# Optimization experiments

Measured on AMD Instinct MI355X. Metric: run time of the kernel, lower is better.

## Reference

```python
import jax, jax.numpy as jnp
import numpy as np

N_NODES = 100000
N_EDGES = 3200000
D_IN = 128
D_OUT = 128
LN_EPS = 1e-5


def setup_inputs() -> dict:
    key = jax.random.key(0)
    k1, k2, k3, k4 = jax.random.split(key, 4)
    x = jax.random.normal(k1, (N_NODES, D_IN), dtype=jnp.float32)
    edge_index = jax.random.randint(k2, (2, N_EDGES), 0, N_NODES, dtype=jnp.int64)
    edge_weight = jax.random.uniform(k3, (N_EDGES,), dtype=jnp.float32)
    W = jax.random.normal(k4, (D_IN, D_OUT), dtype=jnp.float32) * (1.0 / np.sqrt(D_IN))
    b = jnp.zeros((D_OUT,), dtype=jnp.float32)
    gamma = jnp.ones((D_OUT,), dtype=jnp.float32)
    beta = jnp.zeros((D_OUT,), dtype=jnp.float32)
    return {"x": x, "edge_index": edge_index, "edge_weight": edge_weight,
            "W": W, "b": b, "gamma": gamma, "beta": beta}


def _gcn_layer(x, edge_index, edge_weight, W, b, gamma, beta):
    n = x.shape[0]
    row, col = edge_index[0], edge_index[1]  # source -> target
    # add self-loops with weight 1 (PyG GCNConv default)
    loop = jnp.arange(n, dtype=edge_index.dtype)
    row_f = jnp.concatenate([row, loop])
    col_f = jnp.concatenate([col, loop])
    w_f = jnp.concatenate([edge_weight, jnp.ones((n,), dtype=edge_weight.dtype)])
    # symmetric normalization: deg^-1/2[row] * w * deg^-1/2[col]
    deg = jax.ops.segment_sum(w_f, col_f, num_segments=n)
    dis = jnp.where(deg > 0, jax.lax.rsqrt(jnp.maximum(deg, 1e-30)), 0.0)
    norm = dis[row_f] * w_f * dis[col_f]  # [E+N]
    # linear transform first (cheaper), then gather/scatter-add over edges
    h = x @ W  # [N, D_OUT]
    msgs = norm[:, None] * h[row_f]  # [E+N, D_OUT]
    agg = jax.ops.segment_sum(msgs, col_f, num_segments=n) + b
    # LayerNorm over features
    mu = jnp.mean(agg, axis=-1, keepdims=True)
    var = jnp.mean(jnp.square(agg - mu), axis=-1, keepdims=True)
    normed = (agg - mu) * jax.lax.rsqrt(var + LN_EPS) * gamma + beta
    # ReLU; dropout is identity in eval mode
    return jax.nn.relu(normed)


def reference(x, edge_index, edge_weight, W, b, gamma, beta):
    return _gcn_layer(x, edge_index, edge_weight, W, b, gamma, beta)
```

## Files before the change

kernel.cpp:

```cpp
#include <hip/hip_runtime.h>

#define LN_EPS 1e-5f
#define FIX_SCALE 33554432.0f
#define FIX_INV   (1.0f / 33554432.0f)
#define MASK40    ((1ULL << 40) - 1)

__device__ __forceinline__ unsigned pack_bf16x2(float lo, float hi) {
    unsigned a = __float_as_uint(lo), b = __float_as_uint(hi);
    a = (a + 0x7FFFu + ((a >> 16) & 1u)) >> 16;
    b = (b + 0x7FFFu + ((b >> 16) & 1u)) >> 16;
    return a | (b << 16);
}

__device__ __forceinline__ float2 unpack_bf16x2(unsigned u) {
    return make_float2(__uint_as_float(u << 16), __uint_as_float(u & 0xFFFF0000u));
}


__global__ __launch_bounds__(256) void init_packed(unsigned long long* __restrict__ packed, int n) {
    int i = blockIdx.x * 256 + threadIdx.x;
    if (i < n) packed[i] = (1ULL << 25);
}


__global__ __launch_bounds__(256) void hist_edges_rank(const int* __restrict__ ei,
                                                       const float* __restrict__ w,
                                                       unsigned long long* __restrict__ packed,
                                                       unsigned short* __restrict__ rank, int E) {
    int e = blockIdx.x * 256 + threadIdx.x;
    if (e >= E) return;
    int c = ei[(long long)E + e];
    unsigned long long inc = (1ULL << 40) | (unsigned long long)(w[e] * FIX_SCALE + 0.5f);
    unsigned long long old = atomicAdd(&packed[c], inc);
    rank[e] = (unsigned short)(old >> 40);
}

__global__ __launch_bounds__(256) void hist_edges_plain(const int* __restrict__ ei,
                                                        const float* __restrict__ w,
                                                        unsigned long long* __restrict__ packed, int E) {
    int e = blockIdx.x * 256 + threadIdx.x;
    if (e >= E) return;
    int c = ei[(long long)E + e];
    unsigned long long inc = (1ULL << 40) | (unsigned long long)(w[e] * FIX_SCALE + 0.5f);
    atomicAdd(&packed[c], inc);
}


__global__ __launch_bounds__(256) void deg_to_dis(const unsigned long long* __restrict__ packed,
                                                  float* __restrict__ dis, int n) {
    int i = blockIdx.x * 256 + threadIdx.x;
    if (i < n) {
        float d = (float)(packed[i] & MASK40) * FIX_INV;
        dis[i] = rsqrtf(fmaxf(d, 1e-30f));
    }
}


__global__ __launch_bounds__(256) void scan_bsums(const unsigned long long* __restrict__ packed,
                                                  int* __restrict__ bsum, int n) {
    int base = blockIdx.x * 1024;
    int t = threadIdx.x;
    int s = 0;
    #pragma unroll
    for (int k = 0; k < 4; k++) {
        int i = base + t * 4 + k;
        if (i < n) s += (int)(packed[i] >> 40);
    }
    #pragma unroll
    for (int off = 32; off; off >>= 1) s += __shfl_xor(s, off);
    __shared__ int wsum[4];
    if ((t & 63) == 0) wsum[t >> 6] = s;
    __syncthreads();
    if (t == 0) bsum[blockIdx.x] = wsum[0] + wsum[1] + wsum[2] + wsum[3];
}

__global__ __launch_bounds__(256) void scan_boff(const int* __restrict__ bsum,
                                                 int* __restrict__ boff, int B,
                                                 int* __restrict__ rp, int n, int E) {
    int t = threadIdx.x;
    int v[4]; int loc = 0;
    #pragma unroll
    for (int k = 0; k < 4; k++) {
        int i = t * 4 + k;
        v[k] = (i < B) ? bsum[i] : 0;
        loc += v[k];
    }
    int lane = t & 63, wv = t >> 6;
    int incl = loc;
    #pragma unroll
    for (int off = 1; off < 64; off <<= 1) {
        int tt = __shfl_up(incl, off);
        if (lane >= off) incl += tt;
    }
    __shared__ int wsum[4];
    if (lane == 63) wsum[wv] = incl;
    __syncthreads();
    int woff = 0;
    for (int k = 0; k < wv; k++) woff += wsum[k];
    int run = woff + incl - loc;
    #pragma unroll
    for (int k = 0; k < 4; k++) {
        int i = t * 4 + k;
        if (i < B) boff[i] = run;
        run += v[k];
    }
    if (t == 0) rp[n] = E;
}

__global__ __launch_bounds__(256) void scan_write(const unsigned long long* __restrict__ packed,
                                                  const int* __restrict__ boff,
                                                  int* __restrict__ rp, int n) {
    int base = blockIdx.x * 1024;
    int t = threadIdx.x;
    int v[4]; int loc = 0;
    #pragma unroll
    for (int k = 0; k < 4; k++) {
        int i = base + t * 4 + k;
        v[k] = (i < n) ? (int)(packed[i] >> 40) : 0;
        loc += v[k];
    }
    int lane = t & 63, wv = t >> 6;
    int incl = loc;
    #pragma unroll
    for (int off = 1; off < 64; off <<= 1) {
        int tt = __shfl_up(incl, off);
        if (lane >= off) incl += tt;
    }
    __shared__ int wsum[4];
    if (lane == 63) wsum[wv] = incl;
    __syncthreads();
    int woff = 0;
    for (int k = 0; k < wv; k++) woff += wsum[k];
    int run = boff[blockIdx.x] + woff + incl - loc;
    #pragma unroll
    for (int k = 0; k < 4; k++) {
        int i = base + t * 4 + k;
        if (i < n) { rp[i] = run; run += v[k]; }
    }
}


__global__ __launch_bounds__(256) void sort_edges_rank(const int* __restrict__ ei,
                                                       const float* __restrict__ w,
                                                       const float* __restrict__ dis,
                                                       const int* __restrict__ rp,
                                                       const unsigned short* __restrict__ rank,
                                                       int2* __restrict__ es, int E) {
    int e = blockIdx.x * 256 + threadIdx.x;
    if (e >= E) return;
    int r = ei[e], c = ei[(long long)E + e];
    int pos = rp[c] + (int)rank[e];
    es[pos] = make_int2(r, __float_as_int(dis[r] * w[e]));
}

__global__ __launch_bounds__(256) void sort_edges_cursor(const int* __restrict__ ei,
                                                         const float* __restrict__ w,
                                                         const float* __restrict__ dis,
                                                         const int* __restrict__ rp,
                                                         int* __restrict__ cursor,
                                                         int2* __restrict__ es, int E) {
    int e = blockIdx.x * 256 + threadIdx.x;
    if (e >= E) return;
    int r = ei[e], c = ei[(long long)E + e];
    int pos = rp[c] + atomicAdd(&cursor[c], 1);
    es[pos] = make_int2(r, __float_as_int(dis[r] * w[e]));
}


__global__ __launch_bounds__(256) void gemm_xw(const float* __restrict__ x,
                                               const float* __restrict__ W,
                                               unsigned* __restrict__ hb, int n) {
    __shared__ float xt[128][64];
    __shared__ float Ws[128][64];
    const int tid = threadIdx.x;
    const int brow = blockIdx.x * 64;
    const int chalf = blockIdx.y;

    for (int i = tid; i < 64 * 32; i += 256) {
        int r = i >> 5, c4 = i & 31, k0 = c4 * 4;
        int gr = brow + r;
        float4 v = make_float4(0.f, 0.f, 0.f, 0.f);
        if (gr < n) v = *(const float4*)(x + (size_t)gr * 128 + k0);
        xt[k0 + 0][r] = v.x; xt[k0 + 1][r] = v.y;
        xt[k0 + 2][r] = v.z; xt[k0 + 3][r] = v.w;
    }
    for (int i = tid; i < 128 * 16; i += 256) {
        int k = i >> 4, c4 = i & 15;
        float4 v = *(const float4*)(W + (size_t)k * 128 + chalf * 64 + c4 * 4);
        *(float4*)&Ws[k][c4 * 4] = v;
    }
    __syncthreads();

    const int r0 = (tid >> 4) * 4;
    const int c0 = (tid & 15) * 4;
    float4 acc0 = make_float4(0, 0, 0, 0), acc1 = acc0, acc2 = acc0, acc3 = acc0;
    #pragma unroll 8
    for (int k = 0; k < 128; k++) {
        float4 xa = *(const float4*)&xt[k][r0];
        float4 wb = *(const float4*)&Ws[k][c0];
        acc0.x += xa.x * wb.x; acc0.y += xa.x * wb.y; acc0.z += xa.x * wb.z; acc0.w += xa.x * wb.w;
        acc1.x += xa.y * wb.x; acc1.y += xa.y * wb.y; acc1.z += xa.y * wb.z; acc1.w += xa.y * wb.w;
        acc2.x += xa.z * wb.x; acc2.y += xa.z * wb.y; acc2.z += xa.z * wb.z; acc2.w += xa.z * wb.w;
        acc3.x += xa.w * wb.x; acc3.y += xa.w * wb.y; acc3.z += xa.w * wb.z; acc3.w += xa.w * wb.w;
    }
    float4 accs[4] = {acc0, acc1, acc2, acc3};
    #pragma unroll
    for (int i = 0; i < 4; i++) {
        int gr = brow + r0 + i;
        if (gr < n) {
            uint2 p;
            p.x = pack_bf16x2(accs[i].x, accs[i].y);
            p.y = pack_bf16x2(accs[i].z, accs[i].w);
            *(uint2*)(hb + (size_t)gr * 64 + (chalf * 64 + c0) / 2) = p;
        }
    }
}


__global__ __launch_bounds__(256) void agg_ln(const int* __restrict__ rp,
                                              const int2* __restrict__ es,
                                              const unsigned* __restrict__ hb,
                                              const float* __restrict__ dis,
                                              const float* __restrict__ b,
                                              const float* __restrict__ gamma,
                                              const float* __restrict__ beta,
                                              float* __restrict__ out, int n) {
    const int wave = threadIdx.x >> 6;
    const int lane = threadIdx.x & 63;
    const int node = blockIdx.x * 4 + wave;
    if (node >= n) return;

    const int j0 = rp[node], j1 = rp[node + 1];
    const float ds = dis[node];

    float2 hs = unpack_bf16x2(hb[(size_t)node * 64 + lane]);
    float ax = ds * hs.x, ay = ds * hs.y;

    int j = j0;
    for (; j + 7 < j1; j += 8) {
        int2 ee[8]; unsigned uu[8];
        #pragma unroll
        for (int k = 0; k < 8; k++) ee[k] = es[j + k];
        #pragma unroll
        for (int k = 0; k < 8; k++) uu[k] = hb[(size_t)ee[k].x * 64 + lane];
        #pragma unroll
        for (int k = 0; k < 8; k++) {
            float c = __int_as_float(ee[k].y);
            float2 v = unpack_bf16x2(uu[k]);
            ax += c * v.x;
            ay += c * v.y;
        }
    }
    for (; j < j1; ++j) {
        int2 e0 = es[j];
        float2 v = unpack_bf16x2(hb[(size_t)e0.x * 64 + lane]);
        float c = __int_as_float(e0.y);
        ax += c * v.x;
        ay += c * v.y;
    }

    float2 bb = ((const float2*)b)[lane];
    float vx = ds * ax + bb.x;
    float vy = ds * ay + bb.y;

    float s = vx + vy;
    #pragma unroll
    for (int off = 32; off; off >>= 1) s += __shfl_xor(s, off);
    float mu = s * (1.0f / 128.0f);
    float dx = vx - mu, dy = vy - mu;
    float q = dx * dx + dy * dy;
    #pragma unroll
    for (int off = 32; off; off >>= 1) q += __shfl_xor(q, off);
    float rs = rsqrtf(q * (1.0f / 128.0f) + LN_EPS);

    float2 g = ((const float2*)gamma)[lane], be = ((const float2*)beta)[lane];
    float2 o;
    o.x = fmaxf(dx * rs * g.x + be.x, 0.f);
    o.y = fmaxf(dy * rs * g.y + be.y, 0.f);
    ((float2*)(out + (size_t)node * 128))[lane] = o;
}


extern "C" void kernel_launch(void* const* d_in, const int* in_sizes, int n_in,
                              void* d_out, int out_size, void* d_ws, size_t ws_size,
                              hipStream_t stream) {
    const float* x     = (const float*)d_in[0];
    const int*   ei    = (const int*)d_in[1];
    const float* ew    = (const float*)d_in[2];
    const float* W     = (const float*)d_in[3];
    const float* b     = (const float*)d_in[4];
    const float* gamma = (const float*)d_in[5];
    const float* beta  = (const float*)d_in[6];

    const int n = in_sizes[0] / 128;
    const int E = in_sizes[2];
    float* out = (float*)d_out;

    char* ws = (char*)d_ws;
    const size_t MB = 1u << 20;

    unsigned long long* packed = (unsigned long long*)(ws);
    float* dis  = (float*)(ws + 1 * MB);
    int*   rp   = (int*)(ws + 1 * MB + 512 * 1024);
    int*   bsum = (int*)(ws + 2 * MB);
    int*   boff = (int*)(ws + 2 * MB + 64 * 1024);

    const int B = (n + 1023) / 1024;

    size_t esA_off = 10 * MB;
    size_t hA_off  = esA_off + (size_t)E * 8;
    size_t needA   = hA_off + (size_t)n * 128 * 2;
    size_t esB_off = 3 * MB;
    size_t hB_off  = esB_off + (size_t)E * 8;

    init_packed<<<(n + 255) / 256, 256, 0, stream>>>(packed, n);

    if (ws_size >= needA) {
        unsigned short* rank = (unsigned short*)(ws + 3 * MB);
        int2*     es = (int2*)(ws + esA_off);
        unsigned* hb = (unsigned*)(ws + hA_off);

        hist_edges_rank<<<(E + 255) / 256, 256, 0, stream>>>(ei, ew, packed, rank, E);
        deg_to_dis<<<(n + 255) / 256, 256, 0, stream>>>(packed, dis, n);
        scan_bsums<<<B, 256, 0, stream>>>(packed, bsum, n);
        scan_boff<<<1, 256, 0, stream>>>(bsum, boff, B, rp, n, E);
        scan_write<<<B, 256, 0, stream>>>(packed, boff, rp, n);
        sort_edges_rank<<<(E + 255) / 256, 256, 0, stream>>>(ei, ew, dis, rp, rank, es, E);

        dim3 ggrid((n + 63) / 64, 2);
        gemm_xw<<<ggrid, 256, 0, stream>>>(x, W, hb, n);
        agg_ln<<<(n + 3) / 4, 256, 0, stream>>>(rp, es, hb, dis, b, gamma, beta, out, n);
    } else {
        int*      cursor = (int*)(ws + 2 * MB + 256 * 1024);
        int2*     es = (int2*)(ws + esB_off);
        unsigned* hb = (unsigned*)(ws + hB_off);

        hipMemsetAsync(cursor, 0, (size_t)n * sizeof(int), stream);
        hist_edges_plain<<<(E + 255) / 256, 256, 0, stream>>>(ei, ew, packed, E);
        deg_to_dis<<<(n + 255) / 256, 256, 0, stream>>>(packed, dis, n);
        scan_bsums<<<B, 256, 0, stream>>>(packed, bsum, n);
        scan_boff<<<1, 256, 0, stream>>>(bsum, boff, B, rp, n, E);
        scan_write<<<B, 256, 0, stream>>>(packed, boff, rp, n);
        sort_edges_cursor<<<(E + 255) / 256, 256, 0, stream>>>(ei, ew, dis, rp, cursor, es, E);

        dim3 ggrid((n + 63) / 64, 2);
        gemm_xw<<<ggrid, 256, 0, stream>>>(x, W, hb, n);
        agg_ln<<<(n + 3) / 4, 256, 0, stream>>>(rp, es, hb, dis, b, gamma, beta, out, n);
    }
}
```

Baseline: 577.5 us.

## Co-schedule GEMM with edge histogram in one launch; fuse deg-to-dis into scan

Merges the edge histogram kernel and the x@W GEMM into a single launch where the first blocks do the histogram and the rest do GEMM tiles, so the compute-bound GEMM can overlap with the atomic-bound histogram. It also folds the degree-to-inverse-sqrt computation into the block-sum scan kernel, dropping a launch and a pass over the packed array. The hist blocks now carry 64KB of static shared memory they never use, which may limit their occupancy, and GEMM blocks may start only after most hist blocks are scheduled.

Measured after the change: 556.3 us. 3.7% less time.

```diff
diff --git a/kernel.cpp b/kernel.cpp
--- a/kernel.cpp
+++ b/kernel.cpp
@@ -23,16 +23,71 @@
 }
 
 
-__global__ __launch_bounds__(256) void hist_edges_rank(const int* __restrict__ ei,
-                                                       const float* __restrict__ w,
-                                                       unsigned long long* __restrict__ packed,
-                                                       unsigned short* __restrict__ rank, int E) {
-    int e = blockIdx.x * 256 + threadIdx.x;
-    if (e >= E) return;
-    int c = ei[(long long)E + e];
-    unsigned long long inc = (1ULL << 40) | (unsigned long long)(w[e] * FIX_SCALE + 0.5f);
-    unsigned long long old = atomicAdd(&packed[c], inc);
-    rank[e] = (unsigned short)(old >> 40);
+__global__ __launch_bounds__(256) void gemm_hist(const float* __restrict__ x,
+                                                 const float* __restrict__ W,
+                                                 unsigned* __restrict__ hb, int n,
+                                                 const int* __restrict__ ei,
+                                                 const float* __restrict__ ew,
+                                                 unsigned long long* __restrict__ packed,
+                                                 unsigned short* __restrict__ rank,
+                                                 int E, int histBlocks) {
+    __shared__ float xt[128][64];
+    __shared__ float Ws[128][64];
+    const int tid = threadIdx.x;
+
+    if ((int)blockIdx.x < histBlocks) {
+        int e = blockIdx.x * 256 + tid;
+        if (e < E) {
+            int c = ei[(long long)E + e];
+            unsigned long long inc = (1ULL << 40) | (unsigned long long)(ew[e] * FIX_SCALE + 0.5f);
+            unsigned long long old = atomicAdd(&packed[c], inc);
+            rank[e] = (unsigned short)(old >> 40);
+        }
+        return;
+    }
+
+    const int g = (int)blockIdx.x - histBlocks;
+    const int brow = (g >> 1) * 64;
+    const int chalf = g & 1;
+
+    for (int i = tid; i < 64 * 32; i += 256) {
+        int r = i >> 5, c4 = i & 31, k0 = c4 * 4;
+        int gr = brow + r;
+        float4 v = make_float4(0.f, 0.f, 0.f, 0.f);
+        if (gr < n) v = *(const float4*)(x + (size_t)gr * 128 + k0);
+        xt[k0 + 0][r] = v.x; xt[k0 + 1][r] = v.y;
+        xt[k0 + 2][r] = v.z; xt[k0 + 3][r] = v.w;
+    }
+    for (int i = tid; i < 128 * 16; i += 256) {
+        int k = i >> 4, c4 = i & 15;
+        float4 v = *(const float4*)(W + (size_t)k * 128 + chalf * 64 + c4 * 4);
+        *(float4*)&Ws[k][c4 * 4] = v;
+    }
+    __syncthreads();
+
+    const int r0 = (tid >> 4) * 4;
+    const int c0 = (tid & 15) * 4;
+    float4 acc0 = make_float4(0, 0, 0, 0), acc1 = acc0, acc2 = acc0, acc3 = acc0;
+    #pragma unroll 8
+    for (int k = 0; k < 128; k++) {
+        float4 xa = *(const float4*)&xt[k][r0];
+        float4 wb = *(const float4*)&Ws[k][c0];
+        acc0.x += xa.x * wb.x; acc0.y += xa.x * wb.y; acc0.z += xa.x * wb.z; acc0.w += xa.x * wb.w;
+        acc1.x += xa.y * wb.x; acc1.y += xa.y * wb.y; acc1.z += xa.y * wb.z; acc1.w += xa.y * wb.w;
+        acc2.x += xa.z * wb.x; acc2.y += xa.z * wb.y; acc2.z += xa.z * wb.z; acc2.w += xa.z * wb.w;
+        acc3.x += xa.w * wb.x; acc3.y += xa.w * wb.y; acc3.z += xa.w * wb.z; acc3.w += xa.w * wb.w;
+    }
+    float4 accs[4] = {acc0, acc1, acc2, acc3};
+    #pragma unroll
+    for (int i = 0; i < 4; i++) {
+        int gr = brow + r0 + i;
+        if (gr < n) {
+            uint2 p;
+            p.x = pack_bf16x2(accs[i].x, accs[i].y);
+            p.y = pack_bf16x2(accs[i].z, accs[i].w);
+            *(uint2*)(hb + (size_t)gr * 64 + (chalf * 64 + c0) / 2) = p;
+        }
+    }
 }
 
 __global__ __launch_bounds__(256) void hist_edges_plain(const int* __restrict__ ei,
@@ -45,26 +100,71 @@
     atomicAdd(&packed[c], inc);
 }
 
-
-__global__ __launch_bounds__(256) void deg_to_dis(const unsigned long long* __restrict__ packed,
-                                                  float* __restrict__ dis, int n) {
-    int i = blockIdx.x * 256 + threadIdx.x;
-    if (i < n) {
-        float d = (float)(packed[i] & MASK40) * FIX_INV;
-        dis[i] = rsqrtf(fmaxf(d, 1e-30f));
-    }
-}
-
-
-__global__ __launch_bounds__(256) void scan_bsums(const unsigned long long* __restrict__ packed,
-                                                  int* __restrict__ bsum, int n) {
+__global__ __launch_bounds__(256) void gemm_xw(const float* __restrict__ x,
+                                               const float* __restrict__ W,
+                                               unsigned* __restrict__ hb, int n) {
+    __shared__ float xt[128][64];
+    __shared__ float Ws[128][64];
+    const int tid = threadIdx.x;
+    const int brow = blockIdx.x * 64;
+    const int chalf = blockIdx.y;
+
+    for (int i = tid; i < 64 * 32; i += 256) {
+        int r = i >> 5, c4 = i & 31, k0 = c4 * 4;
+        int gr = brow + r;
+        float4 v = make_float4(0.f, 0.f, 0.f, 0.f);
+        if (gr < n) v = *(const float4*)(x + (size_t)gr * 128 + k0);
+        xt[k0 + 0][r] = v.x; xt[k0 + 1][r] = v.y;
+        xt[k0 + 2][r] = v.z; xt[k0 + 3][r] = v.w;
+    }
+    for (int i = tid; i < 128 * 16; i += 256) {
+        int k = i >> 4, c4 = i & 15;
+        float4 v = *(const float4*)(W + (size_t)k * 128 + chalf * 64 + c4 * 4);
+        *(float4*)&Ws[k][c4 * 4] = v;
+    }
+    __syncthreads();
+
+    const int r0 = (tid >> 4) * 4;
+    const int c0 = (tid & 15) * 4;
+    float4 acc0 = make_float4(0, 0, 0, 0), acc1 = acc0, acc2 = acc0, acc3 = acc0;
+    #pragma unroll 8
+    for (int k = 0; k < 128; k++) {
+        float4 xa = *(const float4*)&xt[k][r0];
+        float4 wb = *(const float4*)&Ws[k][c0];
+        acc0.x += xa.x * wb.x; acc0.y += xa.x * wb.y; acc0.z += xa.x * wb.z; acc0.w += xa.x * wb.w;
+        acc1.x += xa.y * wb.x; acc1.y += xa.y * wb.y; acc1.z += xa.y * wb.z; acc1.w += xa.y * wb.w;
+        acc2.x += xa.z * wb.x; acc2.y += xa.z * wb.y; acc2.z += xa.z * wb.z; acc2.w += xa.z * wb.w;
+        acc3.x += xa.w * wb.x; acc3.y += xa.w * wb.y; acc3.z += xa.w * wb.z; acc3.w += xa.w * wb.w;
+    }
+    float4 accs[4] = {acc0, acc1, acc2, acc3};
+    #pragma unroll
+    for (int i = 0; i < 4; i++) {
+        int gr = brow + r0 + i;
+        if (gr < n) {
+            uint2 p;
+            p.x = pack_bf16x2(accs[i].x, accs[i].y);
+            p.y = pack_bf16x2(accs[i].z, accs[i].w);
+            *(uint2*)(hb + (size_t)gr * 64 + (chalf * 64 + c0) / 2) = p;
+        }
+    }
+}
+
+
+__global__ __launch_bounds__(256) void scan_bsums_dis(const unsigned long long* __restrict__ packed,
+                                                      int* __restrict__ bsum,
+                                                      float* __restrict__ dis, int n) {
     int base = blockIdx.x * 1024;
     int t = threadIdx.x;
     int s = 0;
     #pragma unroll
     for (int k = 0; k < 4; k++) {
         int i = base + t * 4 + k;
-        if (i < n) s += (int)(packed[i] >> 40);
+        if (i < n) {
+            unsigned long long p = packed[i];
+            s += (int)(p >> 40);
+            float d = (float)(p & MASK40) * FIX_INV;
+            dis[i] = rsqrtf(fmaxf(d, 1e-30f));
+        }
     }
     #pragma unroll
     for (int off = 32; off; off >>= 1) s += __shfl_xor(s, off);
@@ -164,56 +264,6 @@
     int r = ei[e], c = ei[(long long)E + e];
     int pos = rp[c] + atomicAdd(&cursor[c], 1);
     es[pos] = make_int2(r, __float_as_int(dis[r] * w[e]));
-}
-
-
-__global__ __launch_bounds__(256) void gemm_xw(const float* __restrict__ x,
-                                               const float* __restrict__ W,
-                                               unsigned* __restrict__ hb, int n) {
-    __shared__ float xt[128][64];
-    __shared__ float Ws[128][64];
-    const int tid = threadIdx.x;
-    const int brow = blockIdx.x * 64;
-    const int chalf = blockIdx.y;
-
-    for (int i = tid; i < 64 * 32; i += 256) {
-        int r = i >> 5, c4 = i & 31, k0 = c4 * 4;
-        int gr = brow + r;
-        float4 v = make_float4(0.f, 0.f, 0.f, 0.f);
-        if (gr < n) v = *(const float4*)(x + (size_t)gr * 128 + k0);
-        xt[k0 + 0][r] = v.x; xt[k0 + 1][r] = v.y;
-        xt[k0 + 2][r] = v.z; xt[k0 + 3][r] = v.w;
-    }
-    for (int i = tid; i < 128 * 16; i += 256) {
-        int k = i >> 4, c4 = i & 15;
-        float4 v = *(const float4*)(W + (size_t)k * 128 + chalf * 64 + c4 * 4);
-        *(float4*)&Ws[k][c4 * 4] = v;
-    }
-    __syncthreads();
-
-    const int r0 = (tid >> 4) * 4;
-    const int c0 = (tid & 15) * 4;
-    float4 acc0 = make_float4(0, 0, 0, 0), acc1 = acc0, acc2 = acc0, acc3 = acc0;
-    #pragma unroll 8
-    for (int k = 0; k < 128; k++) {
-        float4 xa = *(const float4*)&xt[k][r0];
-        float4 wb = *(const float4*)&Ws[k][c0];
-        acc0.x += xa.x * wb.x; acc0.y += xa.x * wb.y; acc0.z += xa.x * wb.z; acc0.w += xa.x * wb.w;
-        acc1.x += xa.y * wb.x; acc1.y += xa.y * wb.y; acc1.z += xa.y * wb.z; acc1.w += xa.y * wb.w;
-        acc2.x += xa.z * wb.x; acc2.y += xa.z * wb.y; acc2.z += xa.z * wb.z; acc2.w += xa.z * wb.w;
-        acc3.x += xa.w * wb.x; acc3.y += xa.w * wb.y; acc3.z += xa.w * wb.z; acc3.w += xa.w * wb.w;
-    }
-    float4 accs[4] = {acc0, acc1, acc2, acc3};
-    #pragma unroll
-    for (int i = 0; i < 4; i++) {
-        int gr = brow + r0 + i;
-        if (gr < n) {
-            uint2 p;
-            p.x = pack_bf16x2(accs[i].x, accs[i].y);
-            p.y = pack_bf16x2(accs[i].z, accs[i].w);
-            *(uint2*)(hb + (size_t)gr * 64 + (chalf * 64 + c0) / 2) = p;
-        }
-    }
 }
 
 
@@ -320,15 +370,16 @@
         int2*     es = (int2*)(ws + esA_off);
         unsigned* hb = (unsigned*)(ws + hA_off);
 
-        hist_edges_rank<<<(E + 255) / 256, 256, 0, stream>>>(ei, ew, packed, rank, E);
-        deg_to_dis<<<(n + 255) / 256, 256, 0, stream>>>(packed, dis, n);
-        scan_bsums<<<B, 256, 0, stream>>>(packed, bsum, n);
+        const int histBlocks = (E + 255) / 256;
+        const int gemmBlocks = ((n + 63) / 64) * 2;
+        gemm_hist<<<histBlocks + gemmBlocks, 256, 0, stream>>>(
+            x, W, hb, n, ei, ew, packed, rank, E, histBlocks);
+
+        scan_bsums_dis<<<B, 256, 0, stream>>>(packed, bsum, dis, n);
         scan_boff<<<1, 256, 0, stream>>>(bsum, boff, B, rp, n, E);
         scan_write<<<B, 256, 0, stream>>>(packed, boff, rp, n);
         sort_edges_rank<<<(E + 255) / 256, 256, 0, stream>>>(ei, ew, dis, rp, rank, es, E);
 
-        dim3 ggrid((n + 63) / 64, 2);
-        gemm_xw<<<ggrid, 256, 0, stream>>>(x, W, hb, n);
         agg_ln<<<(n + 3) / 4, 256, 0, stream>>>(rp, es, hb, dis, b, gamma, beta, out, n);
     } else {
         int*      cursor = (int*)(ws + 2 * MB + 256 * 1024);
@@ -337,8 +388,7 @@
 
         hipMemsetAsync(cursor, 0, (size_t)n * sizeof(int), stream);
         hist_edges_plain<<<(E + 255) / 256, 256, 0, stream>>>(ei, ew, packed, E);
-        deg_to_dis<<<(n + 255) / 256, 256, 0, stream>>>(packed, dis, n);
-        scan_bsums<<<B, 256, 0, stream>>>(packed, bsum, n);
+        scan_bsums_dis<<<B, 256, 0, stream>>>(packed, bsum, dis, n);
         scan_boff<<<1, 256, 0, stream>>>(bsum, boff, B, rp, n, E);
         scan_write<<<B, 256, 0, stream>>>(packed, boff, rp, n);
         sort_edges_cursor<<<(E + 255) / 256, 256, 0, stream>>>(ei, ew, dis, rp, cursor, es, E);
```
